# Kernel tuning notes

Measured on AMD Instinct MI355X. Metric: run time of the kernel, lower is better.

## Reference

```python
import jax, jax.numpy as jnp
import numpy as np

TEMPERATURE = 1.0
BETA = 0.5
# D4 elements in the original enumeration order: [(k, flip) for flip in (False, True) for k in (0,1,2,3)]
ELEMENTS = [(k, f) for f in (False, True) for k in (0, 1, 2, 3)]


def _act(x, k, flip):
    y = jnp.flip(x, axis=-1) if flip else x
    k = k % 4
    if k:
        y = jnp.rot90(y, k, axes=(-2, -1))  # same convention as torch.rot90(dims=(-2,-1))
    return y


def setup_inputs() -> dict:
    key = jax.random.key(0)
    kx, kt = jax.random.split(key)
    x = jax.random.normal(kx, (16, 192, 224, 224), dtype=jnp.float32)
    theta = jax.random.normal(kt, (8,), dtype=jnp.float32)
    return {"x": x, "theta": theta}


def reference(x, theta):
    # weights over the 8 group elements
    w = jax.nn.softmax(theta / TEMPERATURE)
    y = jnp.zeros_like(x)
    for i, (k, f) in enumerate(ELEMENTS):  # fixed loop over 8 group elements
        y = y + w[i] * _act(x, k, f)
    # original divides by the detached running sum of used weights
    w_sum = jax.lax.stop_gradient(jnp.sum(w))
    y = y / jnp.maximum(w_sum, 1e-12)
    # residual mix
    return (1.0 - BETA) * x + BETA * y
```

## Files before the change

### kernel.cpp

```cpp
#include <hip/hip_runtime.h>
#include <hip/hip_bf16.h>

#define N 224
#define TS 32
#define NT 7
#define PITCH 33

__global__ void popmi_coeff_kernel(const float* __restrict__ theta,
                                   float* __restrict__ coef) {
    if (threadIdx.x == 0) {
        float m = theta[0];
        #pragma unroll
        for (int i = 1; i < 8; ++i) m = fmaxf(m, theta[i]);
        float e[8];
        float S = 0.f;
        #pragma unroll
        for (int i = 0; i < 8; ++i) { e[i] = expf(theta[i] - m); S += e[i]; }
        float w[8];
        float ws = 0.f;
        #pragma unroll
        for (int i = 0; i < 8; ++i) { w[i] = e[i] / S; ws += w[i]; }
        const float s = 0.5f / fmaxf(ws, 1e-12f);
        #pragma unroll
        for (int i = 0; i < 8; ++i) coef[i] = s * w[i];
        coef[0] += 0.5f;
    }
}

__global__ __launch_bounds__(256, 4) void popmi_orbit_kernel(
        const float* __restrict__ x, const float* __restrict__ coef,
        float* __restrict__ out) {
    __shared__ float lds[8][TS * PITCH];

    const int bid = blockIdx.x;
    const int p   = bid / 10;
    const int o   = bid - p * 10;

    const int OI[10]  = {0,0,1, 0,1,2, 0,1,2, 3};
    const int OJ[10]  = {1,2,2, 3,3,3, 0,1,2, 3};
    const int ONH[10] = {8,8,8, 4,4,4, 4,4,4, 1};

    const int I = OI[o], J = OJ[o], nH = ONH[o];
    const int rI = NT - 1 - I, rJ = NT - 1 - J;

    const int TI[8] = { I,  J, rI, rJ,  I,  J, rI, rJ };
    const int TJ[8] = { J, rI, rJ,  I, rJ,  I,  J, rI };

    const float* plane  = x   + (size_t)p * (N * N);
    float*       oplane = out + (size_t)p * (N * N);

    const int tid = threadIdx.x;
    const int row = tid >> 3;
    const int cg  = (tid & 7) << 2;

    float c[8];
    #pragma unroll
    for (int g = 0; g < 8; ++g) c[g] = coef[g];

    #pragma unroll
    for (int u = 0; u < 8; ++u) {
        const float4 v = *reinterpret_cast<const float4*>(
            plane + (size_t)(TI[u] * TS + row) * N + TJ[u] * TS + cg);
        float* dst = &lds[u][row * PITCH + cg];
        dst[0] = v.x; dst[1] = v.y; dst[2] = v.z; dst[3] = v.w;
    }
    __syncthreads();

    const int comp[8][8] = {
        {0,1,2,3,4,5,6,7},
        {1,2,3,0,7,4,5,6},
        {2,3,0,1,6,7,4,5},
        {3,0,1,2,5,6,7,4},
        {4,5,6,7,0,1,2,3},
        {5,6,7,4,3,0,1,2},
        {6,7,4,5,2,3,0,1},
        {7,4,5,6,1,2,3,0},
    };

    const int ti  = row;
    const int rti = TS - 1 - ti;

    #pragma unroll
    for (int h = 0; h < 8; ++h) {
        if (h < nH) {
            float res[4];
            #pragma unroll
            for (int q = 0; q < 4; ++q) {
                const int tj  = cg + q;
                const int rtj = TS - 1 - tj;
                res[q] =
                    c[0] * lds[comp[0][h]][ti  * PITCH + tj ] +
                    c[1] * lds[comp[1][h]][tj  * PITCH + rti] +
                    c[2] * lds[comp[2][h]][rti * PITCH + rtj] +
                    c[3] * lds[comp[3][h]][rtj * PITCH + ti ] +
                    c[4] * lds[comp[4][h]][ti  * PITCH + rtj] +
                    c[5] * lds[comp[5][h]][tj  * PITCH + ti ] +
                    c[6] * lds[comp[6][h]][rti * PITCH + tj ] +
                    c[7] * lds[comp[7][h]][rtj * PITCH + rti];
            }
            *reinterpret_cast<float4*>(
                oplane + (size_t)(TI[h] * TS + row) * N + TJ[h] * TS + cg)
                = make_float4(res[0], res[1], res[2], res[3]);
        }
    }
}

extern "C" void kernel_launch(void* const* d_in, const int* in_sizes, int n_in,
                              void* d_out, int out_size, void* d_ws, size_t ws_size,
                              hipStream_t stream) {
    const float* x     = (const float*)d_in[0];
    const float* theta = (const float*)d_in[1];
    float* out  = (float*)d_out;
    float* coef = (float*)d_ws;

    const int planes = in_sizes[0] / (N * N);
    popmi_coeff_kernel<<<1, 64, 0, stream>>>(theta, coef);
    popmi_orbit_kernel<<<planes * 10, 256, 0, stream>>>(x, coef, out);
}
```

Measured before the change: 261.5 us.

## Fuse softmax into orbit kernel and load only distinct tiles per orbit type

Folds the coefficient computation into the main kernel, so every block computes the softmax itself and the separate launch goes away. Templates the per-orbit work on orbit class so that orbits with 4 or 1 distinct tiles load only those tiles from global memory and remap LDS indices through a canonical table. In the old code every orbit loaded all 8 tiles even when they repeated. This removes redundant global reads on diagonal and center tiles and the branch inside the output loop, at the cost of four template instantiations, larger code, and redundant exp and divide work in every block.

```diff
diff --git a/kernel.cpp b/kernel.cpp
--- a/kernel.cpp
+++ b/kernel.cpp
@@ -6,45 +6,95 @@
 #define NT 7
 #define PITCH 33
 
-__global__ void popmi_coeff_kernel(const float* __restrict__ theta,
-                                   float* __restrict__ coef) {
-    if (threadIdx.x == 0) {
-        float m = theta[0];
+constexpr int COMP[8][8] = {
+    {0,1,2,3,4,5,6,7},
+    {1,2,3,0,7,4,5,6},
+    {2,3,0,1,6,7,4,5},
+    {3,0,1,2,5,6,7,4},
+    {4,5,6,7,0,1,2,3},
+    {5,6,7,4,3,0,1,2},
+    {6,7,4,5,2,3,0,1},
+    {7,4,5,6,1,2,3,0},
+};
+constexpr int CAN[4][8] = {
+    {0,1,2,3,4,5,6,7},
+    {0,1,2,3,0,3,2,1},
+    {0,1,2,3,1,0,3,2},
+    {0,0,0,0,0,0,0,0},
+};
+
+template<int C, int NH, int NU>
+__device__ __forceinline__ void orbit_compute(
+        const float* __restrict__ plane, float* __restrict__ oplane,
+        const float* c, float (*lds)[TS * PITCH],
+        int I, int J, int row, int cg)
+{
+    const int rI = NT - 1 - I, rJ = NT - 1 - J;
+    const int TI[8] = { I,  J, rI, rJ,  I,  J, rI, rJ };
+    const int TJ[8] = { J, rI, rJ,  I, rJ,  I,  J, rI };
+
+    #pragma unroll
+    for (int u = 0; u < NU; ++u) {
+        const float4 v = *reinterpret_cast<const float4*>(
+            plane + (size_t)(TI[u] * TS + row) * N + TJ[u] * TS + cg);
+        float* dst = &lds[u][row * PITCH + cg];
+        dst[0] = v.x; dst[1] = v.y; dst[2] = v.z; dst[3] = v.w;
+    }
+    __syncthreads();
+
+    const int ti = row, rti = TS - 1 - row;
+    #pragma unroll
+    for (int h = 0; h < NH; ++h) {
+        float res[4];
         #pragma unroll
-        for (int i = 1; i < 8; ++i) m = fmaxf(m, theta[i]);
-        float e[8];
-        float S = 0.f;
-        #pragma unroll
-        for (int i = 0; i < 8; ++i) { e[i] = expf(theta[i] - m); S += e[i]; }
-        float w[8];
-        float ws = 0.f;
-        #pragma unroll
-        for (int i = 0; i < 8; ++i) { w[i] = e[i] / S; ws += w[i]; }
-        const float s = 0.5f / fmaxf(ws, 1e-12f);
-        #pragma unroll
-        for (int i = 0; i < 8; ++i) coef[i] = s * w[i];
-        coef[0] += 0.5f;
+        for (int q = 0; q < 4; ++q) {
+            const int tj = cg + q, rtj = TS - 1 - tj;
+            res[q] =
+                c[0] * lds[CAN[C][COMP[0][h]]][ti  * PITCH + tj ] +
+                c[1] * lds[CAN[C][COMP[1][h]]][tj  * PITCH + rti] +
+                c[2] * lds[CAN[C][COMP[2][h]]][rti * PITCH + rtj] +
+                c[3] * lds[CAN[C][COMP[3][h]]][rtj * PITCH + ti ] +
+                c[4] * lds[CAN[C][COMP[4][h]]][ti  * PITCH + rtj] +
+                c[5] * lds[CAN[C][COMP[5][h]]][tj  * PITCH + ti ] +
+                c[6] * lds[CAN[C][COMP[6][h]]][rti * PITCH + tj ] +
+                c[7] * lds[CAN[C][COMP[7][h]]][rtj * PITCH + rti];
+        }
+        *reinterpret_cast<float4*>(
+            oplane + (size_t)(TI[h] * TS + row) * N + TJ[h] * TS + cg)
+            = make_float4(res[0], res[1], res[2], res[3]);
     }
 }
 
-__global__ __launch_bounds__(256, 4) void popmi_orbit_kernel(
-        const float* __restrict__ x, const float* __restrict__ coef,
-        float* __restrict__ out) {
+__global__ __launch_bounds__(256, 4) void popmi_kernel(
+        const float* __restrict__ x, const float* __restrict__ theta,
+        float* __restrict__ out)
+{
     __shared__ float lds[8][TS * PITCH];
+
+    float th[8];
+    #pragma unroll
+    for (int i = 0; i < 8; ++i) th[i] = theta[i];
+    float m = th[0];
+    #pragma unroll
+    for (int i = 1; i < 8; ++i) m = fmaxf(m, th[i]);
+    float e[8], S = 0.f;
+    #pragma unroll
+    for (int i = 0; i < 8; ++i) { e[i] = expf(th[i] - m); S += e[i]; }
+    float w[8], ws = 0.f;
+    #pragma unroll
+    for (int i = 0; i < 8; ++i) { w[i] = e[i] / S; ws += w[i]; }
+    const float s = 0.5f / fmaxf(ws, 1e-12f);
+    float c[8];
+    #pragma unroll
+    for (int i = 0; i < 8; ++i) c[i] = s * w[i];
+    c[0] += 0.5f;
 
     const int bid = blockIdx.x;
     const int p   = bid / 10;
     const int o   = bid - p * 10;
 
-    const int OI[10]  = {0,0,1, 0,1,2, 0,1,2, 3};
-    const int OJ[10]  = {1,2,2, 3,3,3, 0,1,2, 3};
-    const int ONH[10] = {8,8,8, 4,4,4, 4,4,4, 1};
-
-    const int I = OI[o], J = OJ[o], nH = ONH[o];
-    const int rI = NT - 1 - I, rJ = NT - 1 - J;
-
-    const int TI[8] = { I,  J, rI, rJ,  I,  J, rI, rJ };
-    const int TJ[8] = { J, rI, rJ,  I, rJ,  I,  J, rI };
+    const int I = (0x1A211040u >> (3 * o)) & 7;
+    const int J = (0x1A21B691u >> (3 * o)) & 7;
 
     const float* plane  = x   + (size_t)p * (N * N);
     float*       oplane = out + (size_t)p * (N * N);
@@ -53,56 +103,10 @@
     const int row = tid >> 3;
     const int cg  = (tid & 7) << 2;
 
-    float c[8];
-    #pragma unroll
-    for (int g = 0; g < 8; ++g) c[g] = coef[g];
-
-    #pragma unroll
-    for (int u = 0; u < 8; ++u) {
-        const float4 v = *reinterpret_cast<const float4*>(
-            plane + (size_t)(TI[u] * TS + row) * N + TJ[u] * TS + cg);
-        float* dst = &lds[u][row * PITCH + cg];
-        dst[0] = v.x; dst[1] = v.y; dst[2] = v.z; dst[3] = v.w;
-    }
-    __syncthreads();
-
-    const int comp[8][8] = {
-        {0,1,2,3,4,5,6,7},
-        {1,2,3,0,7,4,5,6},
-        {2,3,0,1,6,7,4,5},
-        {3,0,1,2,5,6,7,4},
-        {4,5,6,7,0,1,2,3},
-        {5,6,7,4,3,0,1,2},
-        {6,7,4,5,2,3,0,1},
-        {7,4,5,6,1,2,3,0},
-    };
-
-    const int ti  = row;
-    const int rti = TS - 1 - ti;
-
-    #pragma unroll
-    for (int h = 0; h < 8; ++h) {
-        if (h < nH) {
-            float res[4];
-            #pragma unroll
-            for (int q = 0; q < 4; ++q) {
-                const int tj  = cg + q;
-                const int rtj = TS - 1 - tj;
-                res[q] =
-                    c[0] * lds[comp[0][h]][ti  * PITCH + tj ] +
-                    c[1] * lds[comp[1][h]][tj  * PITCH + rti] +
-                    c[2] * lds[comp[2][h]][rti * PITCH + rtj] +
-                    c[3] * lds[comp[3][h]][rtj * PITCH + ti ] +
-                    c[4] * lds[comp[4][h]][ti  * PITCH + rtj] +
-                    c[5] * lds[comp[5][h]][tj  * PITCH + ti ] +
-                    c[6] * lds[comp[6][h]][rti * PITCH + tj ] +
-                    c[7] * lds[comp[7][h]][rtj * PITCH + rti];
-            }
-            *reinterpret_cast<float4*>(
-                oplane + (size_t)(TI[h] * TS + row) * N + TJ[h] * TS + cg)
-                = make_float4(res[0], res[1], res[2], res[3]);
-        }
-    }
+    if (o < 3)      orbit_compute<0,8,8>(plane, oplane, c, lds, I, J, row, cg);
+    else if (o < 6) orbit_compute<1,4,4>(plane, oplane, c, lds, I, J, row, cg);
+    else if (o < 9) orbit_compute<2,4,4>(plane, oplane, c, lds, I, J, row, cg);
+    else            orbit_compute<3,1,1>(plane, oplane, c, lds, I, J, row, cg);
 }
 
 extern "C" void kernel_launch(void* const* d_in, const int* in_sizes, int n_in,
@@ -110,10 +114,8 @@
                               hipStream_t stream) {
     const float* x     = (const float*)d_in[0];
     const float* theta = (const float*)d_in[1];
-    float* out  = (float*)d_out;
-    float* coef = (float*)d_ws;
+    float* out = (float*)d_out;
 
     const int planes = in_sizes[0] / (N * N);
-    popmi_coeff_kernel<<<1, 64, 0, stream>>>(theta, coef);
-    popmi_orbit_kernel<<<planes * 10, 256, 0, stream>>>(x, coef, out);
+    popmi_kernel<<<planes * 10, 256, 0, stream>>>(x, theta, out);
 }
```

Result: faster. 236.6 us (-9.5%).
